# Optimization experiments

Hardware: AMD Instinct MI355X
Metric: run time of the kernel (lower is better)

## Reference

```python
import jax, jax.numpy as jnp
import numpy as np

EPS = 1e-05


def setup_inputs() -> dict:
    key = jax.random.key(0)
    k1, k2 = jax.random.split(key)
    shape = (4, 1, 192, 192, 192)  # [B, C=1, D, H, W]
    y_pred = jax.random.normal(k1, shape, dtype=jnp.float32)
    y_true = jax.random.normal(k2, shape, dtype=jnp.float32)
    return {"y_pred": y_pred, "y_true": y_true}


def reference(y_pred, y_true):
    # ones-filter conv is exactly a global sum over channel+spatial dims.
    Ii, Ji = y_true, y_pred
    axes = tuple(range(1, Ii.ndim))  # sum over C, D, H, W -> per-batch scalar
    win_size = jnp.asarray(np.prod(Ii.shape[2:]), dtype=Ii.dtype)

    I_sum = jnp.sum(Ii, axis=axes)
    J_sum = jnp.sum(Ji, axis=axes)
    I2_sum = jnp.sum(Ii * Ii, axis=axes)
    J2_sum = jnp.sum(Ji * Ji, axis=axes)
    IJ_sum = jnp.sum(Ii * Ji, axis=axes)

    u_I = I_sum / win_size
    u_J = J_sum / win_size

    cross = IJ_sum - u_J * I_sum - u_I * J_sum + u_I * u_J * win_size
    I_var = I2_sum - 2 * u_I * I_sum + u_I * u_I * win_size
    J_var = J2_sum - 2 * u_J * J_sum + u_J * u_J * win_size

    cc = cross / (jnp.sqrt(I_var) * jnp.sqrt(J_var) + EPS)  # [B]
    # original: reshape to [B, 1] then mean over dim 1 -> [B]
    return cc
```

## Files before the change

kernel.cpp:

```cpp
#include <hip/hip_runtime.h>
#include <math.h>

#define EPS 1e-05

static constexpr int BLOCK = 256;
static constexpr int BPB   = 1024;
static constexpr int NBATCH = 4;
static constexpr long long NPB = 192LL * 192LL * 192LL;

__device__ __forceinline__ double wave_reduce(double v) {
    #pragma unroll
    for (int off = 32; off > 0; off >>= 1)
        v += __shfl_down(v, off, 64);
    return v;
}

__global__ __launch_bounds__(BLOCK) void ncc_partial(
    const float* __restrict__ y_pred, const float* __restrict__ y_true,
    double* __restrict__ part)
{
    const int b = blockIdx.y;
    const float4* I4 = (const float4*)(y_true + (long long)b * NPB);
    const float4* J4 = (const float4*)(y_pred + (long long)b * NPB);
    const long long n4 = NPB / 4;

    double sI = 0.0, sJ = 0.0, sI2 = 0.0, sJ2 = 0.0, sIJ = 0.0;
    for (long long i = (long long)blockIdx.x * BLOCK + threadIdx.x; i < n4;
         i += (long long)BPB * BLOCK) {
        float4 a = I4[i];
        float4 c = J4[i];
        double i0 = a.x, i1 = a.y, i2 = a.z, i3 = a.w;
        double j0 = c.x, j1 = c.y, j2 = c.z, j3 = c.w;
        sI += (i0 + i1) + (i2 + i3);
        sJ += (j0 + j1) + (j2 + j3);
        sI2 = fma(i0, i0, sI2); sI2 = fma(i1, i1, sI2);
        sI2 = fma(i2, i2, sI2); sI2 = fma(i3, i3, sI2);
        sJ2 = fma(j0, j0, sJ2); sJ2 = fma(j1, j1, sJ2);
        sJ2 = fma(j2, j2, sJ2); sJ2 = fma(j3, j3, sJ2);
        sIJ = fma(i0, j0, sIJ); sIJ = fma(i1, j1, sIJ);
        sIJ = fma(i2, j2, sIJ); sIJ = fma(i3, j3, sIJ);
    }

    sI  = wave_reduce(sI);
    sJ  = wave_reduce(sJ);
    sI2 = wave_reduce(sI2);
    sJ2 = wave_reduce(sJ2);
    sIJ = wave_reduce(sIJ);

    __shared__ double lds[BLOCK / 64][5];
    const int wave = threadIdx.x >> 6;
    const int lane = threadIdx.x & 63;
    if (lane == 0) {
        lds[wave][0] = sI;  lds[wave][1] = sJ;
        lds[wave][2] = sI2; lds[wave][3] = sJ2;
        lds[wave][4] = sIJ;
    }
    __syncthreads();
    if (threadIdx.x == 0) {
        double* p = part + ((long long)b * BPB + blockIdx.x) * 5;
        #pragma unroll
        for (int k = 0; k < 5; ++k)
            p[k] = ((lds[0][k] + lds[1][k]) + (lds[2][k] + lds[3][k]));
    }
}

__global__ __launch_bounds__(BLOCK) void ncc_final(
    const double* __restrict__ part, float* __restrict__ out)
{
    const int b = blockIdx.x;
    double s[5] = {0.0, 0.0, 0.0, 0.0, 0.0};
    for (int i = threadIdx.x; i < BPB; i += BLOCK) {
        const double* p = part + ((long long)b * BPB + i) * 5;
        #pragma unroll
        for (int k = 0; k < 5; ++k) s[k] += p[k];
    }
    #pragma unroll
    for (int k = 0; k < 5; ++k) s[k] = wave_reduce(s[k]);

    __shared__ double lds[BLOCK / 64][5];
    const int wave = threadIdx.x >> 6;
    const int lane = threadIdx.x & 63;
    if (lane == 0) {
        #pragma unroll
        for (int k = 0; k < 5; ++k) lds[wave][k] = s[k];
    }
    __syncthreads();
    if (threadIdx.x == 0) {
        double I_sum = 0, J_sum = 0, I2_sum = 0, J2_sum = 0, IJ_sum = 0;
        #pragma unroll
        for (int w = 0; w < BLOCK / 64; ++w) {
            I_sum  += lds[w][0];
            J_sum  += lds[w][1];
            I2_sum += lds[w][2];
            J2_sum += lds[w][3];
            IJ_sum += lds[w][4];
        }
        const double win = (double)NPB;
        const double u_I = I_sum / win;
        const double u_J = J_sum / win;
        const double cross = IJ_sum - u_J * I_sum - u_I * J_sum + u_I * u_J * win;
        const double I_var = I2_sum - 2.0 * u_I * I_sum + u_I * u_I * win;
        const double J_var = J2_sum - 2.0 * u_J * J_sum + u_J * u_J * win;
        const double cc = cross / (sqrt(I_var) * sqrt(J_var) + EPS);
        out[b] = (float)cc;
    }
}

extern "C" void kernel_launch(void* const* d_in, const int* in_sizes, int n_in,
                              void* d_out, int out_size, void* d_ws, size_t ws_size,
                              hipStream_t stream) {
    const float* y_pred = (const float*)d_in[0];
    const float* y_true = (const float*)d_in[1];
    float* out = (float*)d_out;
    double* part = (double*)d_ws;

    dim3 grid1(BPB, NBATCH);
    ncc_partial<<<grid1, BLOCK, 0, stream>>>(y_pred, y_true, part);
    ncc_final<<<NBATCH, BLOCK, 0, stream>>>(part, out);
}
```

Baseline: 240.4 us.

## Tile partial reduction exactly with fp32 inner sums and double-buffered loads

Replaces the grid-stride loop with a fixed tiling: 432 blocks per batch, each thread handling 16 float4 pairs with no bounds checks, register double-buffered in groups of 4 to keep loads in flight. Per-float4 partial sums are now computed in fp32 and only accumulated into double once per group, which removes most of the FP64 conversions and FMAs. The design relies on 432*256*16*4 matching the 192^3 volume exactly. The fp32 inner sums lose a little precision relative to full-double accumulation.

```diff
diff --git a/kernel.cpp b/kernel.cpp
--- a/kernel.cpp
+++ b/kernel.cpp
@@ -3,10 +3,14 @@
 
 #define EPS 1e-05
 
-static constexpr int BLOCK = 256;
-static constexpr int BPB   = 1024;
+static constexpr int BLOCK  = 256;
+static constexpr int BPB    = 432;
+static constexpr int KPT    = 16;
+static constexpr int GRP    = 4;
 static constexpr int NBATCH = 4;
 static constexpr long long NPB = 192LL * 192LL * 192LL;
+
+typedef float v4f __attribute__((ext_vector_type(4)));
 
 __device__ __forceinline__ double wave_reduce(double v) {
     #pragma unroll
@@ -15,30 +19,50 @@
     return v;
 }
 
-__global__ __launch_bounds__(BLOCK) void ncc_partial(
+__global__ __launch_bounds__(BLOCK, 4) void ncc_partial(
     const float* __restrict__ y_pred, const float* __restrict__ y_true,
     double* __restrict__ part)
 {
-    const int b = blockIdx.y;
-    const float4* I4 = (const float4*)(y_true + (long long)b * NPB);
-    const float4* J4 = (const float4*)(y_pred + (long long)b * NPB);
-    const long long n4 = NPB / 4;
+    const int b  = blockIdx.y;
+    const int bx = blockIdx.x;
+    const v4f* __restrict__ I4 = (const v4f*)(y_true + (long long)b * NPB);
+    const v4f* __restrict__ J4 = (const v4f*)(y_pred + (long long)b * NPB);
+
+    const unsigned base = (unsigned)bx * (BLOCK * KPT) + threadIdx.x;
 
     double sI = 0.0, sJ = 0.0, sI2 = 0.0, sJ2 = 0.0, sIJ = 0.0;
-    for (long long i = (long long)blockIdx.x * BLOCK + threadIdx.x; i < n4;
-         i += (long long)BPB * BLOCK) {
-        float4 a = I4[i];
-        float4 c = J4[i];
-        double i0 = a.x, i1 = a.y, i2 = a.z, i3 = a.w;
-        double j0 = c.x, j1 = c.y, j2 = c.z, j3 = c.w;
-        sI += (i0 + i1) + (i2 + i3);
-        sJ += (j0 + j1) + (j2 + j3);
-        sI2 = fma(i0, i0, sI2); sI2 = fma(i1, i1, sI2);
-        sI2 = fma(i2, i2, sI2); sI2 = fma(i3, i3, sI2);
-        sJ2 = fma(j0, j0, sJ2); sJ2 = fma(j1, j1, sJ2);
-        sJ2 = fma(j2, j2, sJ2); sJ2 = fma(j3, j3, sJ2);
-        sIJ = fma(i0, j0, sIJ); sIJ = fma(i1, j1, sIJ);
-        sIJ = fma(i2, j2, sIJ); sIJ = fma(i3, j3, sIJ);
+
+    v4f a[2][GRP], c[2][GRP];
+    #pragma unroll
+    for (int u = 0; u < GRP; ++u) {
+        a[0][u] = I4[base + u * BLOCK];
+        c[0][u] = J4[base + u * BLOCK];
+    }
+    #pragma unroll
+    for (int g = 0; g < KPT / GRP; ++g) {
+        const int cur = g & 1, nxt = cur ^ 1;
+        if (g < KPT / GRP - 1) {
+            const unsigned o = base + (unsigned)(g + 1) * GRP * BLOCK;
+            #pragma unroll
+            for (int u = 0; u < GRP; ++u) {
+                a[nxt][u] = I4[o + u * BLOCK];
+                c[nxt][u] = J4[o + u * BLOCK];
+            }
+        }
+        #pragma unroll
+        for (int u = 0; u < GRP; ++u) {
+            const v4f av = a[cur][u], cv = c[cur][u];
+            float gI  = (av.x + av.y) + (av.z + av.w);
+            float gJ  = (cv.x + cv.y) + (cv.z + cv.w);
+            float gI2 = fmaf(av.x, av.x, fmaf(av.y, av.y, fmaf(av.z, av.z, av.w * av.w)));
+            float gJ2 = fmaf(cv.x, cv.x, fmaf(cv.y, cv.y, fmaf(cv.z, cv.z, cv.w * cv.w)));
+            float gIJ = fmaf(av.x, cv.x, fmaf(av.y, cv.y, fmaf(av.z, cv.z, av.w * cv.w)));
+            sI  += (double)gI;
+            sJ  += (double)gJ;
+            sI2 += (double)gI2;
+            sJ2 += (double)gJ2;
+            sIJ += (double)gIJ;
+        }
     }
 
     sI  = wave_reduce(sI);
@@ -57,7 +81,7 @@
     }
     __syncthreads();
     if (threadIdx.x == 0) {
-        double* p = part + ((long long)b * BPB + blockIdx.x) * 5;
+        double* p = part + ((long long)b * BPB + bx) * 5;
         #pragma unroll
         for (int k = 0; k < 5; ++k)
             p[k] = ((lds[0][k] + lds[1][k]) + (lds[2][k] + lds[3][k]));
@@ -86,15 +110,12 @@
     }
     __syncthreads();
     if (threadIdx.x == 0) {
-        double I_sum = 0, J_sum = 0, I2_sum = 0, J2_sum = 0, IJ_sum = 0;
-        #pragma unroll
-        for (int w = 0; w < BLOCK / 64; ++w) {
-            I_sum  += lds[w][0];
-            J_sum  += lds[w][1];
-            I2_sum += lds[w][2];
-            J2_sum += lds[w][3];
-            IJ_sum += lds[w][4];
-        }
+        double I_sum  = (lds[0][0] + lds[1][0]) + (lds[2][0] + lds[3][0]);
+        double J_sum  = (lds[0][1] + lds[1][1]) + (lds[2][1] + lds[3][1]);
+        double I2_sum = (lds[0][2] + lds[1][2]) + (lds[2][2] + lds[3][2]);
+        double J2_sum = (lds[0][3] + lds[1][3]) + (lds[2][3] + lds[3][3]);
+        double IJ_sum = (lds[0][4] + lds[1][4]) + (lds[2][4] + lds[3][4]);
+
         const double win = (double)NPB;
         const double u_I = I_sum / win;
         const double u_J = J_sum / win;
```

Result: no change. 241.9 us (+0.6%).
